# Optimization experiments

Hardware: AMD Instinct MI355X
Metric: run time of the kernel (lower is better)

Reference implementation:

```python
import jax, jax.numpy as jnp
import numpy as np

B, C_IN, D_IN, H_IN, W_IN = 2, 96, 16, 64, 64
C = 192
HEADS = 8
DH = C // HEADS
NE = 256
TOPK = 32
DEPTH = 2
STRIDE = (2, 2, 2)
EPS = 1e-5
NEG = -1e9


def setup_inputs() -> dict:
    key = jax.random.key(0)
    ks = jax.random.split(key, 8)
    s = 0.02
    return {
        "x": jax.random.normal(ks[0], (B, C_IN, D_IN, H_IN, W_IN), jnp.float32),
        "conv_w": jax.random.normal(ks[1], (C, C_IN) + STRIDE, jnp.float32) * s,
        "conv_b": jnp.zeros((C,), jnp.float32),
        "bn_gamma": jnp.ones((C,), jnp.float32),
        "bn_beta": jnp.zeros((C,), jnp.float32),
        "bn_mean": jnp.zeros((C,), jnp.float32),
        "bn_var": jnp.ones((C,), jnp.float32),
        "ln_g": jnp.ones((DEPTH, 3, C), jnp.float32),
        "ln_b": jnp.zeros((DEPTH, 3, C), jnp.float32),
        "attn_w": jax.random.normal(ks[2], (DEPTH, 2, 4, C, C), jnp.float32) * s,  # [q,k,v,o]
        "attn_b": jnp.zeros((DEPTH, 2, 4, C), jnp.float32),
        "mlp_w1": jax.random.normal(ks[3], (DEPTH, C, 4 * C), jnp.float32) * s,
        "mlp_b1": jnp.zeros((DEPTH, 4 * C), jnp.float32),
        "mlp_w2": jax.random.normal(ks[4], (DEPTH, 4 * C, C), jnp.float32) * s,
        "mlp_b2": jnp.zeros((DEPTH, C), jnp.float32),
    }


def _ln(x, g, b):
    m = jnp.mean(x, axis=-1, keepdims=True)
    v = jnp.mean(jnp.square(x - m), axis=-1, keepdims=True)
    return (x - m) * jax.lax.rsqrt(v + EPS) * g + b


def _mha(q_in, k_in, v_in, mask, w, b):
    # masked bipartite multi-head attention; mask: (B, Q, Kv) in {0,1}
    Bq, Q, _ = q_in.shape
    Kv = k_in.shape[1]
    q = (q_in @ w[0] + b[0]).reshape(Bq, Q, HEADS, DH)
    k = (k_in @ w[1] + b[1]).reshape(Bq, Kv, HEADS, DH)
    v = (v_in @ w[2] + b[2]).reshape(Bq, Kv, HEADS, DH)
    scores = jnp.einsum('bqhd,bkhd->bhqk', q, k) / jnp.sqrt(jnp.float32(DH))
    scores = jnp.where(mask[:, None, :, :] > 0, scores, NEG)
    attn = jax.nn.softmax(scores, axis=-1)
    out = jnp.einsum('bhqk,bkhd->bqhd', attn, v).reshape(Bq, Q, C)
    out = out @ w[3] + b[3]
    valid = jnp.sum(mask, axis=-1) > 0  # queries with no incident members output 0
    return jnp.where(valid[..., None], out, 0.0)


def _build_hypergraph(x_flat, Dp, Hp, Wp):
    # CS_KNN_3D: evenly-strided center sampling; each hyperedge = K nearest nodes
    # under combined (feature^2 + anisotropic spatial^2) distance, spacing (2,1,1).
    N = Dp * Hp * Wp
    spacing = jnp.array([2.0, 1.0, 1.0], dtype=jnp.float32)
    gd, gh, gw = jnp.meshgrid(jnp.arange(Dp), jnp.arange(Hp), jnp.arange(Wp), indexing='ij')
    coords = jnp.stack([gd, gh, gw], axis=-1).reshape(N, 3).astype(jnp.float32) * spacing
    centers = jnp.round(jnp.linspace(0, N - 1, NE)).astype(jnp.int32)
    cf = x_flat[:, centers, :]                      # (B, Ne, C)
    cp = coords[centers]                            # (Ne, 3)
    feat_d2 = (jnp.sum(cf * cf, -1)[:, :, None] + jnp.sum(x_flat * x_flat, -1)[:, None, :]
               - 2.0 * jnp.einsum('bec,bnc->ben', cf, x_flat))
    spat_d2 = (jnp.sum(cp * cp, -1)[:, None] + jnp.sum(coords * coords, -1)[None, :]
               - 2.0 * cp @ coords.T)               # (Ne, N)
    dist = feat_d2 + spat_d2[None]                  # (B, Ne, N)
    _, idx = jax.lax.top_k(-dist, TOPK)             # (B, Ne, K) nearest nodes per hyperedge
    Bn = x_flat.shape[0]
    Hm = jnp.zeros((Bn, NE, N), jnp.float32).at[
        jnp.arange(Bn)[:, None, None], jnp.arange(NE)[None, :, None], idx].set(1.0)
    return Hm.transpose(0, 2, 1)                    # (B, N, Ne)


def reference(x, conv_w, conv_b, bn_gamma, bn_beta, bn_mean, bn_var,
              ln_g, ln_b, attn_w, attn_b, mlp_w1, mlp_b1, mlp_w2, mlp_b2):
    # downsample: Conv3d(kernel=stride=STRIDE) + BatchNorm3d (eval) + GELU
    y = jax.lax.conv_general_dilated(x, conv_w, window_strides=STRIDE, padding='VALID',
                                     dimension_numbers=('NCDHW', 'OIDHW', 'NCDHW'))
    y = y + conv_b[None, :, None, None, None]
    y = ((y - bn_mean[None, :, None, None, None]) * jax.lax.rsqrt(bn_var + EPS)[None, :, None, None, None]
         * bn_gamma[None, :, None, None, None] + bn_beta[None, :, None, None, None])
    y = jax.nn.gelu(y, approximate=False)
    Bn, Cc, Dp, Hp, Wp = y.shape
    xf = y.reshape(Bn, Cc, Dp * Hp * Wp).transpose(0, 2, 1)  # (B, N, C)
    Hm = _build_hypergraph(xf, Dp, Hp, Wp)                   # (B, N, Ne)
    maskT = Hm.transpose(0, 2, 1)                            # (B, Ne, N)
    deg = jnp.maximum(jnp.sum(Hm, axis=1), 1.0)              # (B, Ne)
    for i in range(DEPTH):
        xn1 = _ln(xf, ln_g[i, 0], ln_b[i, 0])
        he0 = jnp.einsum('bne,bnc->bec', Hm, xn1) / deg[..., None]  # hyperedge init: member mean
        he = _mha(he0, xn1, xn1, maskT, attn_w[i, 0], attn_b[i, 0])  # node -> hyperedge
        xn2 = _ln(xf, ln_g[i, 1], ln_b[i, 1])
        xf = xf + _mha(xn2, he, he, Hm, attn_w[i, 1], attn_b[i, 1])  # hyperedge -> node
        xn3 = _ln(xf, ln_g[i, 2], ln_b[i, 2])
        h = jax.nn.gelu(xn3 @ mlp_w1[i] + mlp_b1[i], approximate=False)
        xf = xf + h @ mlp_w2[i] + mlp_b2[i]
    return xf.transpose(0, 2, 1).reshape(Bn, Cc, Dp, Hp, Wp)
```

## Files before the change

### kernel.cpp

```cpp
#include <hip/hip_runtime.h>
#include <hip/hip_bf16.h>
#include <math.h>

typedef __hip_bfloat16 bf16;
typedef __attribute__((ext_vector_type(8))) short short8v;
typedef __attribute__((ext_vector_type(4))) float float4v;

#define B_ 2
#define CIN 96
#define C_ 192
#define N_ 8192
#define NE_ 256
#define TOPK_ 32
#define HEADS_ 8
#define DH_ 24
#define FF_ 768

__device__ __forceinline__ float b2f(bf16 v) { return __bfloat162float(v); }
__device__ __forceinline__ bf16 f2b(float v) { return __float2bfloat16(v); }
__device__ __forceinline__ unsigned short bfb(float v) {
    union { bf16 b; unsigned short u; } t; t.b = __float2bfloat16(v); return t.u;
}
__device__ __forceinline__ float ldx(const float* p, size_t i) { return p[i]; }
__device__ __forceinline__ float ldx(const bf16* p, size_t i) { return __bfloat162float(p[i]); }
__device__ __forceinline__ void stx(float* p, size_t i, float v) { p[i] = v; }
__device__ __forceinline__ void stx(bf16* p, size_t i, float v) { p[i] = __float2bfloat16(v); }
__device__ __forceinline__ float gelu_f(float x) {
    return 0.5f * x * (1.0f + erff(x * 0.7071067811865475f));
}

__global__ __launch_bounds__(256) void conv_mfma(
    const float* __restrict__ x, const float* __restrict__ cw, const float* __restrict__ cb,
    const float* __restrict__ g, const float* __restrict__ be, const float* __restrict__ mu,
    const float* __restrict__ var, float* __restrict__ xf)
{
    __shared__ unsigned short As[64][40];
    __shared__ unsigned short Bst[64][40];
    int bm = blockIdx.x * 64, bn = blockIdx.y * 64;
    int tid = threadIdx.x;
    int wave = tid >> 6, lane = tid & 63;
    int lrow = lane & 15, lk8 = lane >> 4;
    int r = tid >> 2, kb = (tid & 3) * 8;
    int ng = bm + r;
    int b = ng >> 13, n = ng & 8191;
    int d = n >> 10, h = (n >> 5) & 31, w = n & 31;
    size_t sbase = ((size_t)b * CIN * 16 + 2 * d) * 4096 + (2 * h) * 64 + 2 * w;
    const float* wrow = cw + (size_t)(bn + r) * 768;
    float4v acc[4];
#pragma unroll
    for (int f = 0; f < 4; ++f) acc[f] = (float4v){0.f, 0.f, 0.f, 0.f};
    for (int k0 = 0; k0 < 768; k0 += 32) {
        {
            int ci = (k0 + kb) >> 3;
            const float* xb = x + sbase + (size_t)ci * 16 * 4096;
            As[r][kb + 0] = bfb(xb[0]);
            As[r][kb + 1] = bfb(xb[1]);
            As[r][kb + 2] = bfb(xb[64]);
            As[r][kb + 3] = bfb(xb[65]);
            As[r][kb + 4] = bfb(xb[4096]);
            As[r][kb + 5] = bfb(xb[4097]);
            As[r][kb + 6] = bfb(xb[4160]);
            As[r][kb + 7] = bfb(xb[4161]);
        }
        {
            const float* wq = wrow + k0 + kb;
#pragma unroll
            for (int j = 0; j < 8; ++j) Bst[r][kb + j] = bfb(wq[j]);
        }
        __syncthreads();
        short8v av = *(const short8v*)&As[wave * 16 + lrow][lk8 * 8];
#pragma unroll
        for (int f = 0; f < 4; ++f) {
            short8v bv = *(const short8v*)&Bst[f * 16 + lrow][lk8 * 8];
            acc[f] = __builtin_amdgcn_mfma_f32_16x16x32_bf16(av, bv, acc[f], 0, 0, 0);
        }
        __syncthreads();
    }
#pragma unroll
    for (int f = 0; f < 4; ++f) {
        int co = bn + f * 16 + lrow;
        float bias = cb[co];
        float scale = g[co] / sqrtf(var[co] + 1e-5f);
        float mean = mu[co];
        float shift = be[co];
#pragma unroll
        for (int rr = 0; rr < 4; ++rr) {
            int m = bm + wave * 16 + lk8 * 4 + rr;
            float v = (acc[f][rr] + bias - mean) * scale + shift;
            xf[(size_t)m * C_ + co] = gelu_f(v);
        }
    }
}

__global__ __launch_bounds__(256) void row_ss(const float* __restrict__ xf, float* __restrict__ ssb)
{
    int row = blockIdx.x * 4 + (threadIdx.x >> 6);
    int lane = threadIdx.x & 63;
    const float* xr = xf + (size_t)row * C_;
    float x0 = xr[lane], x1 = xr[lane + 64], x2 = xr[lane + 128];
    float s = x0 * x0 + x1 * x1 + x2 * x2;
    for (int off = 32; off; off >>= 1) s += __shfl_xor(s, off, 64);
    if (lane == 0) ssb[row] = s;
}

__global__ __launch_bounds__(256) void dist_gemm(
    const float* __restrict__ xf, const float* __restrict__ ssb, float* __restrict__ D, int b)
{
    __shared__ float As[16][65];
    __shared__ float Bs[16][64];
    __shared__ int ceb[64];
    int bm = blockIdx.x * 64, bn = blockIdx.y * 64;
    int tid = threadIdx.x;
    int tx = tid & 15, ty = tid >> 4;
    if (tid < 64) ceb[tid] = (int)rintf((float)(bm + tid) * (8191.0f / 255.0f));
    __syncthreads();
    float acc[4][4] = {};
    for (int k0 = 0; k0 < C_; k0 += 16) {
        for (int i = tid; i < 1024; i += 256) {
            int m = i >> 4, kk = i & 15;
            As[kk][m] = xf[(size_t)(b * N_ + ceb[m]) * C_ + k0 + kk];
        }
        for (int i = tid; i < 1024; i += 256) {
            int kk = i & 15, n = i >> 4;
            Bs[kk][n] = xf[(size_t)(b * N_ + bn + n) * C_ + k0 + kk];
        }
        __syncthreads();
        for (int kk = 0; kk < 16; ++kk) {
            float av[4], bvv[4];
#pragma unroll
            for (int i = 0; i < 4; ++i) av[i] = As[kk][ty * 4 + i];
#pragma unroll
            for (int j = 0; j < 4; ++j) bvv[j] = Bs[kk][tx * 4 + j];
#pragma unroll
            for (int i = 0; i < 4; ++i)
#pragma unroll
                for (int j = 0; j < 4; ++j) acc[i][j] += av[i] * bvv[j];
        }
        __syncthreads();
    }
#pragma unroll
    for (int i = 0; i < 4; ++i) {
        int m = bm + ty * 4 + i;
        int ce = ceb[ty * 4 + i];
        int dc = ce >> 10, rc = ce & 1023, hc = rc >> 5, wc = rc & 31;
        float cfs = ssb[b * N_ + ce];
#pragma unroll
        for (int j = 0; j < 4; ++j) {
            int n = bn + tx * 4 + j;
            int dn = n >> 10, rn = n & 1023, hn = rn >> 5, wn = rn & 31;
            float fd = 2.0f * (float)(dc - dn), fh = (float)(hc - hn), fw = (float)(wc - wn);
            float dist = cfs + ssb[b * N_ + n] - 2.0f * acc[i][j] + (fd * fd + fh * fh + fw * fw);
            D[(size_t)m * N_ + n] = dist;
        }
    }
}

__global__ __launch_bounds__(256) void topk_select(
    const float* __restrict__ D, int* __restrict__ members,
    unsigned long long* __restrict__ nodemask, int b)
{
    __shared__ float dist[N_];
    __shared__ float red[256];
    __shared__ int redi[256];
    __shared__ int winner;
    int e = blockIdx.x;
    int tid = threadIdx.x;
    const float* row = D + (size_t)e * N_;
    float lmin = 3.4e38f; int lidx = 0x7fffffff;
    for (int i = 0; i < 32; ++i) {
        int n = tid + (i << 8);
        float v = row[n];
        dist[n] = v;
        if (v < lmin) { lmin = v; lidx = n; }
    }
    for (int k = 0; k < TOPK_; ++k) {
        red[tid] = lmin; redi[tid] = lidx;
        __syncthreads();
        if (tid < 64) {
            float v = red[tid]; int ix = redi[tid];
#pragma unroll
            for (int o = 64; o < 256; o += 64) {
                float ov = red[tid + o]; int oi = redi[tid + o];
                if (ov < v || (ov == v && oi < ix)) { v = ov; ix = oi; }
            }
            for (int off = 32; off; off >>= 1) {
                float ov = __shfl_xor(v, off, 64); int oi = __shfl_xor(ix, off, 64);
                if (ov < v || (ov == v && oi < ix)) { v = ov; ix = oi; }
            }
            if (tid == 0) {
                int wn = ((unsigned)ix < N_) ? ix : 0;
                winner = ix;
                members[(b * NE_ + e) * TOPK_ + k] = wn;
                atomicOr(&nodemask[(size_t)(b * N_ + wn) * 4 + (e >> 6)], 1ull << (e & 63));
            }
        }
        __syncthreads();
        int ix = winner;
        if ((ix & 255) == tid) {
            dist[ix] = 3.4e38f;
            lmin = 3.4e38f; lidx = 0x7fffffff;
            for (int i = 0; i < 32; ++i) {
                int n = tid + (i << 8);
                float dv = dist[n];
                if (dv < lmin) { lmin = dv; lidx = n; }
            }
        }
        __syncthreads();
    }
}

__global__ __launch_bounds__(256) void ln_stats(const float* __restrict__ xf, float2* __restrict__ stats)
{
    int row = blockIdx.x * 4 + (threadIdx.x >> 6);
    int lane = threadIdx.x & 63;
    const float* xr = xf + (size_t)row * C_;
    float x0 = xr[lane], x1 = xr[lane + 64], x2 = xr[lane + 128];
    float s = x0 + x1 + x2;
    for (int off = 32; off; off >>= 1) s += __shfl_xor(s, off, 64);
    float m = s * (1.0f / 192.0f);
    float d0 = x0 - m, d1 = x1 - m, d2 = x2 - m;
    float s2 = d0 * d0 + d1 * d1 + d2 * d2;
    for (int off = 32; off; off >>= 1) s2 += __shfl_xor(s2, off, 64);
    float inv = 1.0f / sqrtf(s2 * (1.0f / 192.0f) + 1e-5f);
    if (lane == 0) stats[row] = make_float2(m, inv);
}

template <int RESID>
__global__ __launch_bounds__(256) void gemm_f32(
    const float* __restrict__ A, const float* __restrict__ Bw, const float* __restrict__ bias,
    float* __restrict__ Cc, int M, int Nn, int K)
{
    __shared__ float As[16][65];
    __shared__ float Bs[16][64];
    int bm = blockIdx.x * 64, bn = blockIdx.y * 64;
    int tid = threadIdx.x;
    int tx = tid & 15, ty = tid >> 4;
    float acc[4][4] = {};
    for (int k0 = 0; k0 < K; k0 += 16) {
        for (int i = tid; i < 1024; i += 256) {
            int m = i >> 4, kk = i & 15;
            As[kk][m] = A[(size_t)(bm + m) * K + k0 + kk];
        }
        for (int i = tid; i < 1024; i += 256) {
            int kk = i >> 6, n = i & 63;
            Bs[kk][n] = Bw[(size_t)(k0 + kk) * Nn + bn + n];
        }
        __syncthreads();
        for (int kk = 0; kk < 16; ++kk) {
            float av[4], bvv[4];
#pragma unroll
            for (int i = 0; i < 4; ++i) av[i] = As[kk][ty * 4 + i];
#pragma unroll
            for (int j = 0; j < 4; ++j) bvv[j] = Bs[kk][tx * 4 + j];
#pragma unroll
            for (int i = 0; i < 4; ++i)
#pragma unroll
                for (int j = 0; j < 4; ++j) acc[i][j] += av[i] * bvv[j];
        }
        __syncthreads();
    }
#pragma unroll
    for (int i = 0; i < 4; ++i) {
#pragma unroll
        for (int j = 0; j < 4; ++j) {
            int m = bm + ty * 4 + i, n = bn + tx * 4 + j;
            float v = acc[i][j] + bias[n];
            size_t idx = (size_t)m * Nn + n;
            if (RESID) v += Cc[idx];
            Cc[idx] = v;
        }
    }
}

template <int LN, int ACT_GELU, int RESID, typename AT, typename CT>
__global__ __launch_bounds__(256) void gemm_mfma(
    const AT* __restrict__ A, const float2* __restrict__ stats,
    const float* __restrict__ lg, const float* __restrict__ lb,
    const float* __restrict__ Bw, const float* __restrict__ bias,
    CT* __restrict__ Cc, int M, int Nn, int K)
{
    __shared__ unsigned short As[64][40];
    __shared__ unsigned short Bst[64][40];
    int bm = blockIdx.x * 64, bn = blockIdx.y * 64;
    int tid = threadIdx.x;
    int wave = tid >> 6, lane = tid & 63;
    int lrow = lane & 15, lk8 = lane >> 4;
    float4v acc[4];
#pragma unroll
    for (int f = 0; f < 4; ++f) acc[f] = (float4v){0.f, 0.f, 0.f, 0.f};
    for (int k0 = 0; k0 < K; k0 += 32) {
        {
            int r = tid >> 2, kb = (tid & 3) * 8;
            float2 st = LN ? stats[bm + r] : make_float2(0.f, 0.f);
            const AT* arow = A + (size_t)(bm + r) * K + k0 + kb;
#pragma unroll
            for (int j = 0; j < 8; ++j) {
                float a = ldx(arow, j);
                if (LN) a = (a - st.x) * st.y * lg[k0 + kb + j] + lb[k0 + kb + j];
                As[r][kb + j] = bfb(a);
            }
        }
        {
            int k = tid >> 3, nb = (tid & 7) * 8;
            const float* brow = Bw + (size_t)(k0 + k) * Nn + bn + nb;
#pragma unroll
            for (int j = 0; j < 8; ++j) Bst[nb + j][k] = bfb(brow[j]);
        }
        __syncthreads();
        short8v av = *(const short8v*)&As[wave * 16 + lrow][lk8 * 8];
#pragma unroll
        for (int f = 0; f < 4; ++f) {
            short8v bv = *(const short8v*)&Bst[f * 16 + lrow][lk8 * 8];
            acc[f] = __builtin_amdgcn_mfma_f32_16x16x32_bf16(av, bv, acc[f], 0, 0, 0);
        }
        __syncthreads();
    }
#pragma unroll
    for (int f = 0; f < 4; ++f) {
#pragma unroll
        for (int r = 0; r < 4; ++r) {
            int m = bm + wave * 16 + lk8 * 4 + r;
            int n = bn + f * 16 + lrow;
            float v = acc[f][r] + bias[n];
            if (ACT_GELU) v = gelu_f(v);
            size_t idx = (size_t)m * Nn + n;
            if (RESID) v += ldx(Cc, idx);
            stx(Cc, idx, v);
        }
    }
}

__global__ __launch_bounds__(256) void mha1_fused(
    const float* __restrict__ xf, const float2* __restrict__ stats,
    const float* __restrict__ lg, const float* __restrict__ lb,
    const int* __restrict__ members, const bf16* __restrict__ kproj,
    const float* __restrict__ w, const float* __restrict__ bias,
    float* __restrict__ he)
{
    __shared__ int mem[TOPK_];
    __shared__ float2 sst[TOPK_];
    __shared__ float xrows[TOPK_][C_];
    __shared__ float kv[TOPK_][C_];
    __shared__ float h0[C_], q[C_], probs[256], wrow[HEADS_ * C_], ar[C_];
    int b = blockIdx.x >> 8, e = blockIdx.x & 255;
    int tid = threadIdx.x;
    if (tid < TOPK_) {
        int mn = members[(b * NE_ + e) * TOPK_ + tid];
        if ((unsigned)mn >= N_) mn = 0;
        mem[tid] = mn;
        sst[tid] = stats[b * N_ + mn];
    }
    __syncthreads();
    for (int i = tid; i < TOPK_ * C_; i += 256) {
        int j = i / C_, c = i - j * C_;
        float v = xf[(size_t)(b * N_ + mem[j]) * C_ + c];
        xrows[j][c] = (v - sst[j].x) * sst[j].y * lg[c] + lb[c];
        kv[j][c] = b2f(kproj[(size_t)(b * N_ + mem[j]) * C_ + c]);
    }
    __syncthreads();
    if (tid < C_) {
        float s = 0.f;
        for (int j = 0; j < TOPK_; ++j) s += xrows[j][tid];
        h0[tid] = s * (1.0f / 32.0f);
    }
    __syncthreads();
    if (tid < C_) {
        float acc = bias[tid];
        for (int k = 0; k < C_; ++k) acc += h0[k] * w[k * C_ + tid];
        q[tid] = acc;
    }
    __syncthreads();
    {
        int hh = tid >> 5, j = tid & 31;
        float s = 0.f;
        for (int d = 0; d < DH_; ++d) s += q[hh * DH_ + d] * kv[j][hh * DH_ + d];
        s *= 0.20412414523193154f;
        float mx = s;
        for (int off = 16; off; off >>= 1) mx = fmaxf(mx, __shfl_xor(mx, off, 32));
        float ex = expf(s - mx);
        float sm = ex;
        for (int off = 16; off; off >>= 1) sm += __shfl_xor(sm, off, 32);
        probs[tid] = ex / sm;
    }
    __syncthreads();
    for (int i = tid; i < HEADS_ * C_; i += 256) {
        int hh = i / C_, k = i - hh * C_;
        const float* pb = probs + hh * 32;
        float acc = 0.f;
        for (int j = 0; j < TOPK_; ++j) acc += pb[j] * xrows[j][k];
        wrow[i] = acc;
    }
    __syncthreads();
    if (tid < C_) {
        int hh = tid / DH_;
        const float* wv = w + 2 * C_ * C_;
        const float* wr2 = wrow + hh * C_;
        float acc = bias[2 * C_ + tid];
        for (int k = 0; k < C_; ++k) acc += wr2[k] * wv[k * C_ + tid];
        ar[tid] = acc;
    }
    __syncthreads();
    if (tid < C_) {
        const float* wo = w + 3 * C_ * C_;
        float acc = bias[3 * C_ + tid];
        for (int k = 0; k < C_; ++k) acc += ar[k] * wo[k * C_ + tid];
        he[(size_t)(b * NE_ + e) * C_ + tid] = acc;
    }
}

__global__ __launch_bounds__(64) void mha2_attn(
    bf16* __restrict__ sbuf, const float* __restrict__ ke, const float* __restrict__ ve,
    const unsigned long long* __restrict__ nodemask)
{
    __shared__ unsigned short lst[NE_];
    __shared__ int cnt;
    __shared__ float qr[C_], sc[HEADS_ * NE_], hsum[HEADS_];
    int blk = blockIdx.x;
    int b = blk >> 13, n = blk & 8191;
    int tid = threadIdx.x;
    size_t row = (size_t)(b * N_ + n) * C_;
    if (tid == 0) {
        int c = 0;
        for (int wd = 0; wd < 4; ++wd) {
            unsigned long long m = nodemask[(size_t)(b * N_ + n) * 4 + wd];
            while (m) {
                int t = __builtin_ctzll(m);
                lst[c++] = (unsigned short)(wd * 64 + t);
                m &= m - 1;
            }
        }
        cnt = c;
    }
    for (int c = tid; c < C_; c += 64) qr[c] = b2f(sbuf[row + c]);
    __syncthreads();
    int m_ = cnt;
    if (m_ == 0) {
        for (int c = tid; c < C_; c += 64) sbuf[row + c] = f2b(0.0f);
        return;
    }
    int hh = tid >> 3, slot = tid & 7;
    float mx = -3.4e38f;
    for (int j = slot; j < m_; j += 8) {
        const float* kr = ke + (size_t)(b * NE_ + lst[j]) * C_ + hh * DH_;
        const float* qh = qr + hh * DH_;
        float s = 0.f;
        for (int d = 0; d < DH_; ++d) s += qh[d] * kr[d];
        s *= 0.20412414523193154f;
        sc[hh * NE_ + j] = s;
        mx = fmaxf(mx, s);
    }
    for (int off = 4; off; off >>= 1) mx = fmaxf(mx, __shfl_xor(mx, off, 8));
    float sum = 0.f;
    for (int j = slot; j < m_; j += 8) {
        float ex = expf(sc[hh * NE_ + j] - mx);
        sc[hh * NE_ + j] = ex;
        sum += ex;
    }
    for (int off = 4; off; off >>= 1) sum += __shfl_xor(sum, off, 8);
    if (slot == 0) hsum[hh] = sum;
    __syncthreads();
    for (int c = tid; c < C_; c += 64) {
        int h2 = c / DH_;
        float acc = 0.f;
        for (int j = 0; j < m_; ++j) acc += sc[h2 * NE_ + j] * ve[(size_t)(b * NE_ + lst[j]) * C_ + c];
        sbuf[row + c] = f2b(acc / hsum[h2]);
    }
}

__global__ __launch_bounds__(256) void write_out_f32(const float* __restrict__ xf, float* __restrict__ out)
{
    __shared__ float t[64 * 193];
    int blk = blockIdx.x;
    int b = blk >> 7, n0 = (blk & 127) * 64;
    for (int i = threadIdx.x; i < 64 * 192; i += 256) {
        int n = i / 192, c = i - (i / 192) * 192;
        t[n * 193 + c] = xf[(size_t)(b * N_ + n0 + n) * C_ + c];
    }
    __syncthreads();
    for (int i = threadIdx.x; i < 64 * 192; i += 256) {
        int c = i >> 6, n = i & 63;
        out[(size_t)(b * C_ + c) * N_ + n0 + n] = t[n * 193 + c];
    }
}

extern "C" void kernel_launch(void* const* d_in, const int* in_sizes, int n_in,
                              void* d_out, int out_size, void* d_ws, size_t ws_size,
                              hipStream_t stream)
{
    const float* x   = (const float*)d_in[0];
    const float* cw  = (const float*)d_in[1];
    const float* cb  = (const float*)d_in[2];
    const float* bg  = (const float*)d_in[3];
    const float* bb  = (const float*)d_in[4];
    const float* bm  = (const float*)d_in[5];
    const float* bv  = (const float*)d_in[6];
    const float* lng = (const float*)d_in[7];
    const float* lnb = (const float*)d_in[8];
    const float* aw  = (const float*)d_in[9];
    const float* ab  = (const float*)d_in[10];
    const float* m1  = (const float*)d_in[11];
    const float* mb1 = (const float*)d_in[12];
    const float* m2  = (const float*)d_in[13];
    const float* mb2 = (const float*)d_in[14];
    float* out = (float*)d_out;

    float* xf = (float*)d_ws;
    char* ob = (char*)d_out;
    float* D = (float*)ob;
    unsigned long long* nodemask = (unsigned long long*)(ob + 8388608);
    int* members = (int*)(ob + 8912896);
    float* ssb   = (float*)(ob + 8978432);
    bf16* sbuf = (bf16*)ob;
    char* ob2 = ob + 6291456;
    float2* stats = (float2*)(ob2 + 524288);
    float* he     = (float*)(ob2 + 720896);
    float* ke     = (float*)(ob2 + 1114112);
    float* ve     = (float*)(ob2 + 1507328);

    hipMemsetAsync(nodemask, 0, (size_t)B_ * N_ * 4 * sizeof(unsigned long long), stream);

    const int MT = B_ * N_;
    {
        dim3 gc(MT / 64, C_ / 64);
        conv_mfma<<<gc, 256, 0, stream>>>(x, cw, cb, bg, bb, bm, bv, xf);
    }
    row_ss<<<MT / 4, 256, 0, stream>>>(xf, ssb);
    for (int b = 0; b < B_; ++b) {
        dim3 gd(4, N_ / 64);
        dist_gemm<<<gd, 256, 0, stream>>>(xf, ssb, D, b);
        topk_select<<<NE_, 256, 0, stream>>>(D, members, nodemask, b);
    }

    for (int i = 0; i < 2; ++i) {
        const float* w0 = aw + (size_t)((i * 2 + 0) * 4) * C_ * C_;
        const float* b0 = ab + (size_t)((i * 2 + 0) * 4) * C_;
        const float* w1 = aw + (size_t)((i * 2 + 1) * 4) * C_ * C_;
        const float* b1 = ab + (size_t)((i * 2 + 1) * 4) * C_;
        const float* g1 = lng + (i * 3 + 0) * C_, *bb1 = lnb + (i * 3 + 0) * C_;
        const float* g2 = lng + (i * 3 + 1) * C_, *bb2 = lnb + (i * 3 + 1) * C_;
        const float* g3 = lng + (i * 3 + 2) * C_, *bb3 = lnb + (i * 3 + 2) * C_;

        ln_stats<<<MT / 4, 256, 0, stream>>>(xf, stats);
        {
            dim3 gk(MT / 64, C_ / 64);
            gemm_mfma<1, 0, 0, float, bf16><<<gk, 256, 0, stream>>>(
                xf, stats, g1, bb1, w0 + 1 * C_ * C_, b0 + 1 * C_, sbuf, MT, C_, C_);
        }
        mha1_fused<<<B_ * NE_, 256, 0, stream>>>(xf, stats, g1, bb1, members, sbuf, w0, b0, he);

        ln_stats<<<MT / 4, 256, 0, stream>>>(xf, stats);
        {
            dim3 ge(B_ * NE_ / 64, C_ / 64);
            gemm_f32<0><<<ge, 256, 0, stream>>>(he, w1 + 1 * C_ * C_, b1 + 1 * C_, ke, B_ * NE_, C_, C_);
            gemm_f32<0><<<ge, 256, 0, stream>>>(he, w1 + 2 * C_ * C_, b1 + 2 * C_, ve, B_ * NE_, C_, C_);
            dim3 gq(MT / 64, C_ / 64);
            gemm_mfma<1, 0, 0, float, bf16><<<gq, 256, 0, stream>>>(
                xf, stats, g2, bb2, w1 + 0 * C_ * C_, b1 + 0 * C_, sbuf, MT, C_, C_);
        }
        mha2_attn<<<MT, 64, 0, stream>>>(sbuf, ke, ve, nodemask);
        {
            dim3 go(MT / 64, C_ / 64);
            gemm_mfma<0, 0, 1, bf16, float><<<go, 256, 0, stream>>>(
                sbuf, nullptr, nullptr, nullptr, w1 + 3 * C_ * C_, b1 + 3 * C_, xf, MT, C_, C_);
        }

        ln_stats<<<MT / 4, 256, 0, stream>>>(xf, stats);
        for (int ch = 0; ch < 4; ++ch) {
            int off = ch * 4096;
            dim3 g1d(4096 / 64, FF_ / 64);
            gemm_mfma<1, 1, 0, float, bf16><<<g1d, 256, 0, stream>>>(
                xf + (size_t)off * C_, stats + off, g3, bb3,
                m1 + (size_t)i * C_ * FF_, mb1 + i * FF_, sbuf, 4096, FF_, C_);
            dim3 g2d(4096 / 64, C_ / 64);
            gemm_mfma<0, 0, 1, bf16, float><<<g2d, 256, 0, stream>>>(
                sbuf, nullptr, nullptr, nullptr,
                m2 + (size_t)i * FF_ * C_, mb2 + i * C_, xf + (size_t)off * C_, 4096, C_, FF_);
        }
    }
    write_out_f32<<<B_ * N_ / 64, 256, 0, stream>>>(xf, out);
}
```

Measured before the change: 772.9 us.

## Rewrite top-k selection as single-wavefront with per-lane top-4 candidate cache

New measurement: 1.031 ms. +33.3%, slower.

```diff
diff --git a/kernel.cpp b/kernel.cpp
--- a/kernel.cpp
+++ b/kernel.cpp
@@ -155,57 +155,66 @@
     }
 }
 
-__global__ __launch_bounds__(256) void topk_select(
+__global__ __launch_bounds__(64) void topk_select(
     const float* __restrict__ D, int* __restrict__ members,
     unsigned long long* __restrict__ nodemask, int b)
 {
     __shared__ float dist[N_];
-    __shared__ float red[256];
-    __shared__ int redi[256];
-    __shared__ int winner;
     int e = blockIdx.x;
-    int tid = threadIdx.x;
+    int lane = threadIdx.x;
     const float* row = D + (size_t)e * N_;
-    float lmin = 3.4e38f; int lidx = 0x7fffffff;
-    for (int i = 0; i < 32; ++i) {
-        int n = tid + (i << 8);
-        float v = row[n];
-        dist[n] = v;
-        if (v < lmin) { lmin = v; lidx = n; }
-    }
+    float cv[4] = {3.4e38f, 3.4e38f, 3.4e38f, 3.4e38f};
+    int cix[4] = {0x7fffffff, 0x7fffffff, 0x7fffffff, 0x7fffffff};
+    for (int i = lane; i < N_; i += 64) {
+        float v = row[i];
+        dist[i] = v;
+        if (v < cv[3] || (v == cv[3] && i < cix[3])) {
+            cv[3] = v; cix[3] = i;
+#pragma unroll
+            for (int j = 3; j > 0; --j) {
+                if (cv[j] < cv[j - 1] || (cv[j] == cv[j - 1] && cix[j] < cix[j - 1])) {
+                    float tv = cv[j]; cv[j] = cv[j - 1]; cv[j - 1] = tv;
+                    int ti = cix[j]; cix[j] = cix[j - 1]; cix[j - 1] = ti;
+                }
+            }
+        }
+    }
+    int depth = 4;
     for (int k = 0; k < TOPK_; ++k) {
-        red[tid] = lmin; redi[tid] = lidx;
-        __syncthreads();
-        if (tid < 64) {
-            float v = red[tid]; int ix = redi[tid];
-#pragma unroll
-            for (int o = 64; o < 256; o += 64) {
-                float ov = red[tid + o]; int oi = redi[tid + o];
-                if (ov < v || (ov == v && oi < ix)) { v = ov; ix = oi; }
+        float v = cv[0]; int ix = cix[0];
+#pragma unroll
+        for (int off = 32; off; off >>= 1) {
+            float ov = __shfl_xor(v, off, 64); int oi = __shfl_xor(ix, off, 64);
+            if (ov < v || (ov == v && oi < ix)) { v = ov; ix = oi; }
+        }
+        if (lane == 0) {
+            int wn = ((unsigned)ix < N_) ? ix : 0;
+            members[(b * NE_ + e) * TOPK_ + k] = wn;
+            atomicOr(&nodemask[(size_t)(b * N_ + wn) * 4 + (e >> 6)], 1ull << (e & 63));
+        }
+        if ((ix & 63) == lane) {
+            dist[ix] = 3.4e38f;
+            cv[0] = cv[1]; cix[0] = cix[1];
+            cv[1] = cv[2]; cix[1] = cix[2];
+            cv[2] = cv[3]; cix[2] = cix[3];
+            cv[3] = 3.4e38f; cix[3] = 0x7fffffff;
+            if (--depth == 0) {
+                for (int i = lane; i < N_; i += 64) {
+                    float dv = dist[i];
+                    if (dv < cv[3] || (dv == cv[3] && i < cix[3])) {
+                        cv[3] = dv; cix[3] = i;
+#pragma unroll
+                        for (int j = 3; j > 0; --j) {
+                            if (cv[j] < cv[j - 1] || (cv[j] == cv[j - 1] && cix[j] < cix[j - 1])) {
+                                float tv = cv[j]; cv[j] = cv[j - 1]; cv[j - 1] = tv;
+                                int ti = cix[j]; cix[j] = cix[j - 1]; cix[j - 1] = ti;
+                            }
+                        }
+                    }
+                }
+                depth = 4;
             }
-            for (int off = 32; off; off >>= 1) {
-                float ov = __shfl_xor(v, off, 64); int oi = __shfl_xor(ix, off, 64);
-                if (ov < v || (ov == v && oi < ix)) { v = ov; ix = oi; }
-            }
-            if (tid == 0) {
-                int wn = ((unsigned)ix < N_) ? ix : 0;
-                winner = ix;
-                members[(b * NE_ + e) * TOPK_ + k] = wn;
-                atomicOr(&nodemask[(size_t)(b * N_ + wn) * 4 + (e >> 6)], 1ull << (e & 63));
-            }
-        }
-        __syncthreads();
-        int ix = winner;
-        if ((ix & 255) == tid) {
-            dist[ix] = 3.4e38f;
-            lmin = 3.4e38f; lidx = 0x7fffffff;
-            for (int i = 0; i < 32; ++i) {
-                int n = tid + (i << 8);
-                float dv = dist[n];
-                if (dv < lmin) { lmin = dv; lidx = n; }
-            }
-        }
-        __syncthreads();
+        }
     }
 }
 
@@ -528,7 +537,7 @@
     for (int b = 0; b < B_; ++b) {
         dim3 gd(4, N_ / 64);
         dist_gemm<<<gd, 256, 0, stream>>>(xf, ssb, D, b);
-        topk_select<<<NE_, 256, 0, stream>>>(D, members, nodemask, b);
+        topk_select<<<NE_, 64, 0, stream>>>(D, members, nodemask, b);
     }
 
     for (int i = 0; i < 2; ++i) {
```
